# Optimization experiments

Measured on AMD Instinct MI355X. Metric: run time of the kernel, lower is better.

Reference implementation:

```python
import jax, jax.numpy as jnp
import numpy as np

N, E = 50000, 800000
D, H, C, ED = 128, 8, 16, 32  # in_channels, heads, head_dim, edge_dim
EPS = 1e-5

def _ln(x, g, b):
    mu = jnp.mean(x, axis=-1, keepdims=True)
    var = jnp.mean((x - mu) ** 2, axis=-1, keepdims=True)
    return (x - mu) * jax.lax.rsqrt(var + EPS) * g + b

def setup_inputs() -> dict:
    key = jax.random.key(0)
    ks = jax.random.split(key, 20)
    s = 0.05
    inp = {
        'x': jax.random.normal(ks[0], (N, D), jnp.float32),
        'edge_index': jax.random.randint(ks[1], (2, E), 0, N, jnp.int64),
        'edge_attr': jax.random.normal(ks[2], (E, ED), jnp.float32),
        'Wq': jax.random.normal(ks[3], (D, H * C)) * s,
        'bq': jnp.zeros((H * C,)),
        'Wk': jax.random.normal(ks[4], (D, H * C)) * s,
        'bk': jnp.zeros((H * C,)),
        'Wv': jax.random.normal(ks[5], (D, H * C)) * s,
        'bv': jnp.zeros((H * C,)),
        'We': jax.random.normal(ks[6], (ED, H * C)) * s,
        'Wskip': jax.random.normal(ks[7], (D, H * C)) * s,
        'bskip': jnp.zeros((H * C,)),
        'ln1_g': jnp.ones((D,)), 'ln1_b': jnp.zeros((D,)),
        'W1': jax.random.normal(ks[8], (D, 4 * D)) * s,
        'b1': jnp.zeros((4 * D,)),
        'W2': jax.random.normal(ks[9], (4 * D, D)) * s,
        'b2': jnp.zeros((D,)),
        'ln2_g': jnp.ones((D,)), 'ln2_b': jnp.zeros((D,)),
    }
    return inp

def reference(x, edge_index, edge_attr, Wq, bq, Wk, bk, Wv, bv, We, Wskip, bskip,
              ln1_g, ln1_b, W1, b1, W2, b2, ln2_g, ln2_b):
    src, dst = edge_index[0], edge_index[1]
    # node-level projections, then gather per-edge  [N,H,C] -> [E,H,C]
    q = (x @ Wq + bq).reshape(N, H, C)
    k = (x @ Wk + bk).reshape(N, H, C)
    v = (x @ Wv + bv).reshape(N, H, C)
    e = (edge_attr @ We).reshape(E, H, C)
    k_e = k[src] + e
    alpha = jnp.sum(q[dst] * k_e, axis=-1) / jnp.sqrt(jnp.float32(C))  # [E,H]
    # segment softmax over destination nodes
    m = jax.ops.segment_max(alpha, dst, num_segments=N)               # [N,H]
    p = jnp.exp(alpha - m[dst])
    denom = jax.ops.segment_sum(p, dst, num_segments=N)
    a = p / (denom[dst] + 1e-16)
    out_e = (v[src] + e) * a[..., None]                               # [E,H,C]
    attn = jax.ops.segment_sum(out_e, dst, num_segments=N).reshape(N, H * C)
    attn = attn + x @ Wskip + bskip  # root/skip connection
    # transformer block: residual + LN + FFN + LN (dropout = identity, eval)
    h = _ln(x + attn, ln1_g, ln1_b)
    ffn = jax.nn.relu(h @ W1 + b1) @ W2 + b2
    return _ln(h + ffn, ln2_g, ln2_b)
```

## Files before the change

### kernel.cpp

```cpp
#include <hip/hip_runtime.h>
#include <hip/hip_bf16.h>

using bf16 = __hip_bfloat16;
typedef __attribute__((ext_vector_type(8))) short short8;
typedef __attribute__((ext_vector_type(4))) float floatx4;

#define NN 50000
#define EE 800000
#define DD 128
#define HH 8
#define CC 16
#define EDD 32
#define DF 512
#define NQC 64
#define PART 782

__device__ __forceinline__ float b2f(bf16 v) { return __bfloat162float(v); }
__device__ __forceinline__ float bs2f(short s) {
    bf16 h = *reinterpret_cast<bf16*>(&s);
    return __bfloat162float(h);
}
__device__ __forceinline__ float bu2f(unsigned short s) {
    unsigned int u = ((unsigned int)s) << 16;
    return *reinterpret_cast<float*>(&u);
}
__device__ __forceinline__ short f2bs(float v) {
    bf16 h = __float2bfloat16(v);
    return *reinterpret_cast<short*>(&h);
}

__global__ void k_detect(const int* __restrict__ ei, int* __restrict__ flag)
{
    if (threadIdx.x == 0 && blockIdx.x == 0) {
        int all0 = 1;
        for (int i = 0; i < 16; ++i) all0 &= (ei[2 * i + 1] == 0);
        flag[0] = all0;
    }
}

__device__ __forceinline__ int clampn(int v)
{
    return (v < 0) ? 0 : (v >= NN ? NN - 1 : v);
}

__global__ void k_packall(const float* __restrict__ Wq, const float* __restrict__ Wk,
                          const float* __restrict__ Wv, const float* __restrict__ Wsk,
                          const float* __restrict__ W1, const float* __restrict__ W2,
                          const float* __restrict__ We,
                          bf16* __restrict__ wqp, bf16* __restrict__ wkp,
                          bf16* __restrict__ wvp, bf16* __restrict__ wskp,
                          bf16* __restrict__ w1p, bf16* __restrict__ w2p,
                          bf16* __restrict__ wep)
{
    int idx = blockIdx.x * 256 + threadIdx.x;
    const float* W; bf16* out; int ksteps, N, local;
    if (idx < 65536) {
        int wsel = idx >> 14; local = idx & 16383;
        W   = (wsel == 0) ? Wq  : (wsel == 1) ? Wk  : (wsel == 2) ? Wv  : Wsk;
        out = (wsel == 0) ? wqp : (wsel == 1) ? wkp : (wsel == 2) ? wvp : wskp;
        ksteps = 4; N = 128;
    } else if (idx < 131072) { local = idx - 65536;  W = W1; out = w1p; ksteps = 4;  N = 512; }
    else if (idx < 196608)   { local = idx - 131072; W = W2; out = w2p; ksteps = 16; N = 128; }
    else if (idx < 200704)   { local = idx - 196608; W = We; out = wep; ksteps = 1;  N = 128; }
    else return;
    int j = local & 7, lane = (local >> 3) & 63, rest = local >> 9;
    int kstep = rest % ksteps, ntile = rest / ksteps;
    int quad = lane >> 4, m = lane & 15;
    int k = kstep * 32 + quad * 8 + j;
    int n = ntile * 16 + m;
    out[local] = __float2bfloat16(W[(size_t)k * N + n]);
}

__global__ __launch_bounds__(256) void k_proj(
    const float* __restrict__ x,
    const bf16* __restrict__ wqp, const bf16* __restrict__ wkp,
    const bf16* __restrict__ wvp, const bf16* __restrict__ wskp,
    const float* __restrict__ bq, const float* __restrict__ bk,
    const float* __restrict__ bv, const float* __restrict__ bsk,
    bf16* __restrict__ qb, unsigned int* __restrict__ kvb,
    bf16* __restrict__ skipb)
{
    __shared__ __align__(16) short xs[32][136];
    __shared__ __align__(16) short os[32][520];
    const int t = threadIdx.x;
    const int wave = t >> 6, lane = t & 63;
    const int quad = lane >> 4, m = lane & 15;
    const int n0 = blockIdx.x * 32;

    for (int idx = t; idx < 32 * 32; idx += 256) {
        int row = idx >> 5, g = idx & 31;
        int node = n0 + row;
        float4 xv = {0.f, 0.f, 0.f, 0.f};
        if (node < NN) xv = *reinterpret_cast<const float4*>(&x[(size_t)node * 128 + g * 4]);
        short4 s4;
        s4.x = f2bs(xv.x); s4.y = f2bs(xv.y); s4.z = f2bs(xv.z); s4.w = f2bs(xv.w);
        *reinterpret_cast<short4*>(&xs[row][g * 4]) = s4;
    }
    __syncthreads();

    const bf16* Wp = (wave == 0) ? wqp : (wave == 1) ? wkp : (wave == 2) ? wvp : wskp;
    const float* bias = (wave == 0) ? bq : (wave == 1) ? bk : (wave == 2) ? bv : bsk;

    floatx4 acc[2][8];
#pragma unroll
    for (int mt = 0; mt < 2; ++mt)
#pragma unroll
        for (int nt = 0; nt < 8; ++nt) acc[mt][nt] = (floatx4){0.f, 0.f, 0.f, 0.f};

#pragma unroll
    for (int kstep = 0; kstep < 4; ++kstep) {
        short8 af0 = *reinterpret_cast<const short8*>(&xs[m][kstep * 32 + quad * 8]);
        short8 af1 = *reinterpret_cast<const short8*>(&xs[16 + m][kstep * 32 + quad * 8]);
#pragma unroll
        for (int nt = 0; nt < 8; ++nt) {
            short8 bf = *reinterpret_cast<const short8*>(
                reinterpret_cast<const short*>(Wp) + ((nt * 4 + kstep) * 64 + lane) * 8);
            acc[0][nt] = __builtin_amdgcn_mfma_f32_16x16x32_bf16(af0, bf, acc[0][nt], 0, 0, 0);
            acc[1][nt] = __builtin_amdgcn_mfma_f32_16x16x32_bf16(af1, bf, acc[1][nt], 0, 0, 0);
        }
    }
#pragma unroll
    for (int nt = 0; nt < 8; ++nt) {
        float bs = bias[nt * 16 + m];
#pragma unroll
        for (int mt = 0; mt < 2; ++mt)
#pragma unroll
            for (int r = 0; r < 4; ++r)
                os[mt * 16 + quad * 4 + r][wave * 128 + nt * 16 + m] = f2bs(acc[mt][nt][r] + bs);
    }
    __syncthreads();
    for (int idx = t; idx < 32 * 64; idx += 256) {
        int row = idx >> 6, c = idx & 63;
        int node = n0 + row;
        if (node >= NN) continue;
        unsigned int qu  = *reinterpret_cast<const unsigned int*>(&os[row][2 * c]);
        unsigned int ku  = *reinterpret_cast<const unsigned int*>(&os[row][128 + 2 * c]);
        unsigned int vu  = *reinterpret_cast<const unsigned int*>(&os[row][256 + 2 * c]);
        unsigned int sku = *reinterpret_cast<const unsigned int*>(&os[row][384 + 2 * c]);
        reinterpret_cast<unsigned int*>(qb)[(size_t)node * 64 + c] = qu;
        reinterpret_cast<unsigned int*>(skipb)[(size_t)node * 64 + c] = sku;
        uint2 kv;
        kv.x = (ku & 0xffffu) | (vu << 16);
        kv.y = (ku >> 16) | (vu & 0xffff0000u);
        reinterpret_cast<uint2*>(kvb)[(size_t)node * 64 + c] = kv;
    }
}

__global__ void k_hist(const int* __restrict__ ei, const int* __restrict__ flag,
                       int* __restrict__ deg)
{
    int tt = blockIdx.x * 256 + threadIdx.x;
    int i0 = tt * 2;
    if (i0 >= EE) return;
    int d0, d1;
    if (flag[0]) {
        int4 v = *reinterpret_cast<const int4*>(&ei[2 * EE + 2 * i0]);
        d0 = v.x; d1 = v.z;
    } else {
        int2 v = *reinterpret_cast<const int2*>(&ei[EE + i0]);
        d0 = v.x; d1 = v.y;
    }
    atomicAdd(&deg[clampn(d0)], 1);
    atomicAdd(&deg[clampn(d1)], 1);
}

__global__ __launch_bounds__(1024) void k_scan(const int* __restrict__ deg,
                                               int* __restrict__ rowstart)
{
    __shared__ int s[1024];
    const int t = threadIdx.x;
    const int CH = 49;
    int base = t * CH;
    int sum = 0;
    for (int i = 0; i < CH; i++) {
        int idx = base + i;
        if (idx < NN) sum += deg[idx];
    }
    s[t] = sum;
    __syncthreads();
    int own = sum;
    for (int off = 1; off < 1024; off <<= 1) {
        int v = (t >= off) ? s[t - off] : 0;
        __syncthreads();
        s[t] += v;
        __syncthreads();
    }
    int run = s[t] - own;
    for (int i = 0; i < CH; i++) {
        int idx = base + i;
        if (idx < NN) {
            rowstart[idx] = run;
            run += deg[idx];
        }
    }
    if (t == 0) rowstart[NN] = EE;
}

__global__ void k_scatter(const int* __restrict__ ei, const int* __restrict__ flag,
                          const int* __restrict__ rowstart,
                          int* __restrict__ cursor, int* __restrict__ srcs,
                          const float* __restrict__ ea,
                          short* __restrict__ eacsr)
{
    int i = blockIdx.x * 256 + threadIdx.x;
    if (i >= EE) return;
    int is64 = flag[0];
    int d = clampn(is64 ? ei[2 * EE + 2 * i] : ei[EE + i]);
    int s = clampn(is64 ? ei[2 * i] : ei[i]);
    int pos = rowstart[d] + atomicAdd(&cursor[d], 1);
    srcs[pos] = s;
    const float4* er = reinterpret_cast<const float4*>(ea + (size_t)i * 32);
    short8* dst = reinterpret_cast<short8*>(eacsr + (size_t)pos * 32);
#pragma unroll
    for (int g = 0; g < 4; ++g) {
        float4 a = er[2 * g], b = er[2 * g + 1];
        short8 o;
        o[0] = f2bs(a.x); o[1] = f2bs(a.y); o[2] = f2bs(a.z); o[3] = f2bs(a.w);
        o[4] = f2bs(b.x); o[5] = f2bs(b.y); o[6] = f2bs(b.z); o[7] = f2bs(b.w);
        dst[g] = o;
    }
}

__global__ __launch_bounds__(256) void k_attn(
    const float* __restrict__ x,
    const short* __restrict__ eacsr, const bf16* __restrict__ wep,
    const bf16* __restrict__ qb, const unsigned int* __restrict__ kvb,
    const bf16* __restrict__ skipb,
    const int* __restrict__ rowstart, const int* __restrict__ srcs,
    const float* __restrict__ ln1g, const float* __restrict__ ln1b,
    int* __restrict__ qcounter, bf16* __restrict__ hb)
{
    __shared__ __align__(16) short es[4][128][18];
    __shared__ __align__(16) short wes[4096];
    const int t = threadIdx.x;
    const int wave = t >> 6, lane = t & 63;
    const int quad = lane >> 4, m = lane & 15;

    for (int idx = t; idx < 512; idx += 256)
        *reinterpret_cast<short8*>(&wes[idx * 8]) =
            *reinterpret_cast<const short8*>(reinterpret_cast<const short*>(wep) + idx * 8);
    __syncthreads();

    short (*esw)[18] = es[wave];
    const float QS = 0.3606737602f;

    const int gw = blockIdx.x * 4 + wave;
    const int c  = gw & (NQC - 1);
    const int base = c * PART;
    const int cnt_c = (NN - base < PART) ? (NN - base) : PART;
    int* qc = qcounter + c * 16;

    for (;;) {
        int nl;
        if (lane == 0) nl = atomicAdd(qc, 1);
        nl = __builtin_amdgcn_readfirstlane(nl);
        if (nl >= cnt_c) break;
        const int n = base + nl;

        unsigned int qp = reinterpret_cast<const unsigned int*>(qb)[(size_t)n * 64 + lane];
        float q0 = bu2f((unsigned short)(qp & 0xffffu)) * QS;
        float q1 = bu2f((unsigned short)(qp >> 16)) * QS;

        const int eoff = rowstart[n], eend = rowstart[n + 1];
        float lsum = 0.f, acc0 = 0.f, acc1 = 0.f;

        for (int p0 = eoff; p0 < eend; p0 += 16) {
            int pos = p0 + m;
            int pc = (pos < eend) ? pos : eoff;
            int sj_all = srcs[pc];

            short8 Af = *reinterpret_cast<const short8*>(eacsr + (size_t)pc * 32 + quad * 8);

            uint2 kvr[16];
#pragma unroll
            for (int j = 0; j < 16; ++j) {
                int sj = __builtin_amdgcn_readlane(sj_all, j);
                kvr[j] = reinterpret_cast<const uint2*>(kvb + (size_t)(unsigned)sj * 128)[lane];
            }

#pragma unroll
            for (int nt = 0; nt < 8; ++nt) {
                short8 Bf = *reinterpret_cast<const short8*>(&wes[(nt * 64 + lane) * 8]);
                floatx4 C = {0.f, 0.f, 0.f, 0.f};
                C = __builtin_amdgcn_mfma_f32_16x16x32_bf16(Af, Bf, C, 0, 0, 0);
                int col = nt * 16 + m;
                unsigned int d0 = (unsigned int)(unsigned short)f2bs(C[0]) |
                                  ((unsigned int)(unsigned short)f2bs(C[1]) << 16);
                unsigned int d1 = (unsigned int)(unsigned short)f2bs(C[2]) |
                                  ((unsigned int)(unsigned short)f2bs(C[3]) << 16);
                unsigned int* p = reinterpret_cast<unsigned int*>(&esw[col][quad * 4]);
                p[0] = d0; p[1] = d1;
            }
            __builtin_amdgcn_wave_barrier();

            unsigned int ea[8], eb[8];
            {
                const unsigned int* ra = reinterpret_cast<const unsigned int*>(&esw[2 * lane][0]);
                const unsigned int* rb = reinterpret_cast<const unsigned int*>(&esw[2 * lane + 1][0]);
#pragma unroll
                for (int jj = 0; jj < 8; ++jj) { ea[jj] = ra[jj]; eb[jj] = rb[jj]; }
            }

            int cnt = eend - p0; if (cnt > 16) cnt = 16;
#pragma unroll
            for (int j = 0; j < 16; ++j) {
                unsigned int eva = ea[j >> 1], evb = eb[j >> 1];
                float e0 = (j & 1) ? bu2f((unsigned short)(eva >> 16))
                                   : bu2f((unsigned short)(eva & 0xffffu));
                float e1 = (j & 1) ? bu2f((unsigned short)(evb >> 16))
                                   : bu2f((unsigned short)(evb & 0xffffu));
                float k0 = bu2f((unsigned short)(kvr[j].x & 0xffffu));
                float v0 = bu2f((unsigned short)(kvr[j].x >> 16));
                float k1 = bu2f((unsigned short)(kvr[j].y & 0xffffu));
                float v1 = bu2f((unsigned short)(kvr[j].y >> 16));
                float pr = fmaf(k1 + e1, q1, (k0 + e0) * q0);
                pr += __shfl_xor(pr, 1);
                pr += __shfl_xor(pr, 2);
                pr += __shfl_xor(pr, 4);
                float w = (j < cnt) ? __builtin_amdgcn_exp2f(pr) : 0.f;
                lsum += w;
                acc0 = fmaf(v0 + e0, w, acc0);
                acc1 = fmaf(v1 + e1, w, acc1);
            }
            __builtin_amdgcn_wave_barrier();
        }

        float rden = 1.f / (lsum + 1e-16f);
        float attn0 = acc0 * rden, attn1 = acc1 * rden;
        float2 xv = *reinterpret_cast<const float2*>(x + (size_t)n * 128 + 2 * lane);
        unsigned int skp = reinterpret_cast<const unsigned int*>(skipb)[(size_t)n * 64 + lane];
        float pre0 = xv.x + attn0 + bu2f((unsigned short)(skp & 0xffffu));
        float pre1 = xv.y + attn1 + bu2f((unsigned short)(skp >> 16));
        float s1 = pre0 + pre1, s2 = pre0 * pre0 + pre1 * pre1;
#pragma unroll
        for (int off = 1; off < 64; off <<= 1) {
            s1 += __shfl_xor(s1, off);
            s2 += __shfl_xor(s2, off);
        }
        float mu = s1 * (1.f / 128.f);
        float var = s2 * (1.f / 128.f) - mu * mu;
        float inv = rsqrtf(var + 1e-5f);
        float2 g  = *reinterpret_cast<const float2*>(ln1g + 2 * lane);
        float2 bb = *reinterpret_cast<const float2*>(ln1b + 2 * lane);
        float h0 = (pre0 - mu) * inv * g.x + bb.x;
        float h1 = (pre1 - mu) * inv * g.y + bb.y;
        unsigned int hu = (unsigned int)(unsigned short)f2bs(h0) |
                          ((unsigned int)(unsigned short)f2bs(h1) << 16);
        reinterpret_cast<unsigned int*>(hb)[(size_t)n * 64 + lane] = hu;
    }
}

__global__ __launch_bounds__(256) void k_ffn(
    const bf16* __restrict__ hb,
    const bf16* __restrict__ w1p, const float* __restrict__ b1,
    const bf16* __restrict__ w2p, const float* __restrict__ b2,
    const float* __restrict__ ln2g, const float* __restrict__ ln2b,
    float* __restrict__ out)
{
    __shared__ __align__(16) short hs[32][136];
    __shared__ __align__(16) short t1s[32][520];
    float* fs = reinterpret_cast<float*>(&t1s[0][0]);
    const int t = threadIdx.x;
    const int wave = t >> 6, lane = t & 63;
    const int quad = lane >> 4, m = lane & 15;
    const int n0 = blockIdx.x * 32;

    for (int idx = t; idx < 32 * 16; idx += 256) {
        int row = idx >> 4, g = idx & 15;
        int node = n0 + row;
        if (node < NN) {
            *reinterpret_cast<float4*>(&hs[row][g * 8]) =
                *reinterpret_cast<const float4*>(&hb[(size_t)node * 128 + g * 8]);
        } else {
            float4 z = {0.f, 0.f, 0.f, 0.f};
            *reinterpret_cast<float4*>(&hs[row][g * 8]) = z;
        }
    }
    __syncthreads();

    floatx4 acc1[2][8];
#pragma unroll
    for (int mt = 0; mt < 2; ++mt)
#pragma unroll
        for (int nt = 0; nt < 8; ++nt) acc1[mt][nt] = (floatx4){0.f, 0.f, 0.f, 0.f};
#pragma unroll
    for (int kstep = 0; kstep < 4; ++kstep) {
        short8 af0 = *reinterpret_cast<const short8*>(&hs[m][kstep * 32 + quad * 8]);
        short8 af1 = *reinterpret_cast<const short8*>(&hs[16 + m][kstep * 32 + quad * 8]);
#pragma unroll
        for (int nt = 0; nt < 8; ++nt) {
            short8 bf = *reinterpret_cast<const short8*>(
                reinterpret_cast<const short*>(w1p) + (((wave * 8 + nt) * 4 + kstep) * 64 + lane) * 8);
            acc1[0][nt] = __builtin_amdgcn_mfma_f32_16x16x32_bf16(af0, bf, acc1[0][nt], 0, 0, 0);
            acc1[1][nt] = __builtin_amdgcn_mfma_f32_16x16x32_bf16(af1, bf, acc1[1][nt], 0, 0, 0);
        }
    }
#pragma unroll
    for (int nt = 0; nt < 8; ++nt) {
        float bs = b1[wave * 128 + nt * 16 + m];
#pragma unroll
        for (int mt = 0; mt < 2; ++mt)
#pragma unroll
            for (int r = 0; r < 4; ++r)
                t1s[mt * 16 + quad * 4 + r][wave * 128 + nt * 16 + m] =
                    f2bs(fmaxf(acc1[mt][nt][r] + bs, 0.f));
    }
    __syncthreads();

    floatx4 acc2[2][2];
#pragma unroll
    for (int mt = 0; mt < 2; ++mt)
#pragma unroll
        for (int nt = 0; nt < 2; ++nt) acc2[mt][nt] = (floatx4){0.f, 0.f, 0.f, 0.f};
#pragma unroll
    for (int kstep = 0; kstep < 16; ++kstep) {
        short8 af0 = *reinterpret_cast<const short8*>(&t1s[m][kstep * 32 + quad * 8]);
        short8 af1 = *reinterpret_cast<const short8*>(&t1s[16 + m][kstep * 32 + quad * 8]);
#pragma unroll
        for (int nt = 0; nt < 2; ++nt) {
            short8 bf = *reinterpret_cast<const short8*>(
                reinterpret_cast<const short*>(w2p) + (((wave * 2 + nt) * 16 + kstep) * 64 + lane) * 8);
            acc2[0][nt] = __builtin_amdgcn_mfma_f32_16x16x32_bf16(af0, bf, acc2[0][nt], 0, 0, 0);
            acc2[1][nt] = __builtin_amdgcn_mfma_f32_16x16x32_bf16(af1, bf, acc2[1][nt], 0, 0, 0);
        }
    }
    __syncthreads();
#pragma unroll
    for (int nt = 0; nt < 2; ++nt) {
        int col = (wave * 2 + nt) * 16 + m;
        float bs = b2[col];
#pragma unroll
        for (int mt = 0; mt < 2; ++mt)
#pragma unroll
            for (int r = 0; r < 4; ++r)
                fs[(mt * 16 + quad * 4 + r) * 132 + col] = acc2[mt][nt][r] + bs;
    }
    __syncthreads();

    for (int rr = 0; rr < 8; ++rr) {
        int row = wave * 8 + rr;
        int node = n0 + row;
        float p0 = bs2f(hs[row][lane]) + fs[row * 132 + lane];
        float p1 = bs2f(hs[row][lane + 64]) + fs[row * 132 + lane + 64];
        float s1 = p0 + p1, s2 = p0 * p0 + p1 * p1;
#pragma unroll
        for (int off = 1; off < 64; off <<= 1) {
            s1 += __shfl_xor(s1, off);
            s2 += __shfl_xor(s2, off);
        }
        float mu = s1 * (1.f / 128.f);
        float var = s2 * (1.f / 128.f) - mu * mu;
        float inv = rsqrtf(var + 1e-5f);
        if (node < NN) {
            out[(size_t)node * 128 + lane] = (p0 - mu) * inv * ln2g[lane] + ln2b[lane];
            out[(size_t)node * 128 + lane + 64] = (p1 - mu) * inv * ln2g[lane + 64] + ln2b[lane + 64];
        }
    }
}

extern "C" void kernel_launch(void* const* d_in, const int* in_sizes, int n_in,
                              void* d_out, int out_size, void* d_ws, size_t ws_size,
                              hipStream_t stream)
{
    const float* x    = (const float*)d_in[0];
    const int*   ei   = (const int*)d_in[1];
    const float* ea   = (const float*)d_in[2];
    const float* Wq   = (const float*)d_in[3];
    const float* bq   = (const float*)d_in[4];
    const float* Wk   = (const float*)d_in[5];
    const float* bk   = (const float*)d_in[6];
    const float* Wv   = (const float*)d_in[7];
    const float* bv   = (const float*)d_in[8];
    const float* We   = (const float*)d_in[9];
    const float* Wsk  = (const float*)d_in[10];
    const float* bsk  = (const float*)d_in[11];
    const float* ln1g = (const float*)d_in[12];
    const float* ln1b = (const float*)d_in[13];
    const float* W1   = (const float*)d_in[14];
    const float* b1   = (const float*)d_in[15];
    const float* W2   = (const float*)d_in[16];
    const float* b2   = (const float*)d_in[17];
    const float* ln2g = (const float*)d_in[18];
    const float* ln2b = (const float*)d_in[19];

    char* ws = (char*)d_ws;
    size_t off = 0;
    auto alloc = [&](size_t bytes) -> void* {
        void* p = ws + off;
        off += (bytes + 255) & ~(size_t)255;
        return p;
    };
    int*   flag     = (int*)alloc(256);
    int*   qcounter = (int*)alloc((size_t)NQC * 16 * 4);
    int*   deg      = (int*)alloc((size_t)NN * 4);
    int*   cursor   = (int*)alloc((size_t)NN * 4);
    int*   rowstart = (int*)alloc((size_t)(NN + 1) * 4);
    int*   srcs     = (int*)alloc((size_t)EE * 4);
    short* eacsr    = (short*)alloc((size_t)EE * 32 * 2);
    bf16*  qb       = (bf16*)alloc((size_t)NN * 128 * 2);
    unsigned int* kvb = (unsigned int*)alloc((size_t)NN * 128 * 4);
    bf16*  skipb    = (bf16*)alloc((size_t)NN * 128 * 2);
    bf16*  hb       = (bf16*)alloc((size_t)NN * 128 * 2);
    bf16*  wqp      = (bf16*)alloc((size_t)16384 * 2);
    bf16*  wkp      = (bf16*)alloc((size_t)16384 * 2);
    bf16*  wvp      = (bf16*)alloc((size_t)16384 * 2);
    bf16*  wskp     = (bf16*)alloc((size_t)16384 * 2);
    bf16*  w1p      = (bf16*)alloc((size_t)65536 * 2);
    bf16*  w2p      = (bf16*)alloc((size_t)65536 * 2);
    bf16*  wep      = (bf16*)alloc((size_t)4096 * 2);

    hipMemsetAsync(deg, 0, (size_t)NN * 4, stream);
    hipMemsetAsync(cursor, 0, (size_t)NN * 4, stream);
    hipMemsetAsync(qcounter, 0, (size_t)NQC * 16 * 4, stream);

    k_detect<<<1, 64, 0, stream>>>(ei, flag);
    k_packall<<<(200704 + 255) / 256, 256, 0, stream>>>(
        Wq, Wk, Wv, Wsk, W1, W2, We, wqp, wkp, wvp, wskp, w1p, w2p, wep);
    k_hist<<<(EE / 2 + 255) / 256, 256, 0, stream>>>(ei, flag, deg);
    k_proj<<<(NN + 31) / 32, 256, 0, stream>>>(x, wqp, wkp, wvp, wskp,
                                               bq, bk, bv, bsk, qb, kvb, skipb);
    k_scan<<<1, 1024, 0, stream>>>(deg, rowstart);
    k_scatter<<<(EE + 255) / 256, 256, 0, stream>>>(ei, flag, rowstart, cursor,
                                                    srcs, ea, eacsr);
    k_attn<<<1536, 256, 0, stream>>>(x, eacsr, wep, qb, kvb, skipb,
                                     rowstart, srcs, ln1g, ln1b, qcounter, hb);
    k_ffn<<<(NN + 31) / 32, 256, 0, stream>>>(hb, w1p, b1, w2p, b2, ln2g, ln2b, (float*)d_out);
}
```

Measured before the change: 564.3 us.

## Fuse detect into pack kernel, batch attention node grabs, use nontemporal stores

Moves the edge-index dtype detection into the weight pack kernel, dropping one kernel launch. The attention kernel now claims four nodes per atomic instead of one, which cuts contention on the per-chunk work counter. The head-reduction shuffles are replaced with ds_swizzle. Nontemporal stores are used for the CSR scatter and for the final output writes. Coarser node grabs may worsen load balance at the tail, and nontemporal stores can hurt if the scattered data is reread soon while still in cache.

```diff
diff --git a/kernel.cpp b/kernel.cpp
--- a/kernel.cpp
+++ b/kernel.cpp
@@ -29,15 +29,6 @@
     return *reinterpret_cast<short*>(&h);
 }
 
-__global__ void k_detect(const int* __restrict__ ei, int* __restrict__ flag)
-{
-    if (threadIdx.x == 0 && blockIdx.x == 0) {
-        int all0 = 1;
-        for (int i = 0; i < 16; ++i) all0 &= (ei[2 * i + 1] == 0);
-        flag[0] = all0;
-    }
-}
-
 __device__ __forceinline__ int clampn(int v)
 {
     return (v < 0) ? 0 : (v >= NN ? NN - 1 : v);
@@ -50,7 +41,8 @@
                           bf16* __restrict__ wqp, bf16* __restrict__ wkp,
                           bf16* __restrict__ wvp, bf16* __restrict__ wskp,
                           bf16* __restrict__ w1p, bf16* __restrict__ w2p,
-                          bf16* __restrict__ wep)
+                          bf16* __restrict__ wep,
+                          const int* __restrict__ ei, int* __restrict__ flag)
 {
     int idx = blockIdx.x * 256 + threadIdx.x;
     const float* W; bf16* out; int ksteps, N, local;
@@ -62,7 +54,14 @@
     } else if (idx < 131072) { local = idx - 65536;  W = W1; out = w1p; ksteps = 4;  N = 512; }
     else if (idx < 196608)   { local = idx - 131072; W = W2; out = w2p; ksteps = 16; N = 128; }
     else if (idx < 200704)   { local = idx - 196608; W = We; out = wep; ksteps = 1;  N = 128; }
-    else return;
+    else {
+        if (idx == 200704) {
+            int all0 = 1;
+            for (int i = 0; i < 16; ++i) all0 &= (ei[2 * i + 1] == 0);
+            flag[0] = all0;
+        }
+        return;
+    }
     int j = local & 7, lane = (local >> 3) & 63, rest = local >> 9;
     int kstep = rest % ksteps, ntile = rest / ksteps;
     int quad = lane >> 4, m = lane & 15;
@@ -208,7 +207,7 @@
     int d = clampn(is64 ? ei[2 * EE + 2 * i] : ei[EE + i]);
     int s = clampn(is64 ? ei[2 * i] : ei[i]);
     int pos = rowstart[d] + atomicAdd(&cursor[d], 1);
-    srcs[pos] = s;
+    __builtin_nontemporal_store(s, &srcs[pos]);
     const float4* er = reinterpret_cast<const float4*>(ea + (size_t)i * 32);
     short8* dst = reinterpret_cast<short8*>(eacsr + (size_t)pos * 32);
 #pragma unroll
@@ -217,7 +216,7 @@
         short8 o;
         o[0] = f2bs(a.x); o[1] = f2bs(a.y); o[2] = f2bs(a.z); o[3] = f2bs(a.w);
         o[4] = f2bs(b.x); o[5] = f2bs(b.y); o[6] = f2bs(b.z); o[7] = f2bs(b.w);
-        dst[g] = o;
+        __builtin_nontemporal_store(o, &dst[g]);
     }
 }
 
@@ -252,101 +251,105 @@
 
     for (;;) {
         int nl;
-        if (lane == 0) nl = atomicAdd(qc, 1);
+        if (lane == 0) nl = atomicAdd(qc, 4);
         nl = __builtin_amdgcn_readfirstlane(nl);
         if (nl >= cnt_c) break;
-        const int n = base + nl;
-
-        unsigned int qp = reinterpret_cast<const unsigned int*>(qb)[(size_t)n * 64 + lane];
-        float q0 = bu2f((unsigned short)(qp & 0xffffu)) * QS;
-        float q1 = bu2f((unsigned short)(qp >> 16)) * QS;
-
-        const int eoff = rowstart[n], eend = rowstart[n + 1];
-        float lsum = 0.f, acc0 = 0.f, acc1 = 0.f;
-
-        for (int p0 = eoff; p0 < eend; p0 += 16) {
-            int pos = p0 + m;
-            int pc = (pos < eend) ? pos : eoff;
-            int sj_all = srcs[pc];
-
-            short8 Af = *reinterpret_cast<const short8*>(eacsr + (size_t)pc * 32 + quad * 8);
-
-            uint2 kvr[16];
-#pragma unroll
-            for (int j = 0; j < 16; ++j) {
-                int sj = __builtin_amdgcn_readlane(sj_all, j);
-                kvr[j] = reinterpret_cast<const uint2*>(kvb + (size_t)(unsigned)sj * 128)[lane];
+        const int nhi = (nl + 4 < cnt_c) ? nl + 4 : cnt_c;
+
+        for (int ni = nl; ni < nhi; ++ni) {
+            const int n = base + ni;
+
+            unsigned int qp = reinterpret_cast<const unsigned int*>(qb)[(size_t)n * 64 + lane];
+            float q0 = bu2f((unsigned short)(qp & 0xffffu)) * QS;
+            float q1 = bu2f((unsigned short)(qp >> 16)) * QS;
+
+            const int eoff = rowstart[n], eend = rowstart[n + 1];
+            float lsum = 0.f, acc0 = 0.f, acc1 = 0.f;
+
+            for (int p0 = eoff; p0 < eend; p0 += 16) {
+                int pos = p0 + m;
+                int pc = (pos < eend) ? pos : eoff;
+                int sj_all = srcs[pc];
+
+                short8 Af = *reinterpret_cast<const short8*>(eacsr + (size_t)pc * 32 + quad * 8);
+
+                uint2 kvr[16];
+#pragma unroll
+                for (int j = 0; j < 16; ++j) {
+                    int sj = __builtin_amdgcn_readlane(sj_all, j);
+                    kvr[j] = reinterpret_cast<const uint2*>(kvb + (size_t)(unsigned)sj * 128)[lane];
+                }
+
+#pragma unroll
+                for (int nt = 0; nt < 8; ++nt) {
+                    short8 Bf = *reinterpret_cast<const short8*>(&wes[(nt * 64 + lane) * 8]);
+                    floatx4 C = {0.f, 0.f, 0.f, 0.f};
+                    C = __builtin_amdgcn_mfma_f32_16x16x32_bf16(Af, Bf, C, 0, 0, 0);
+                    int col = nt * 16 + m;
+                    unsigned int d0 = (unsigned int)(unsigned short)f2bs(C[0]) |
+                                      ((unsigned int)(unsigned short)f2bs(C[1]) << 16);
+                    unsigned int d1 = (unsigned int)(unsigned short)f2bs(C[2]) |
+                                      ((unsigned int)(unsigned short)f2bs(C[3]) << 16);
+                    unsigned int* p = reinterpret_cast<unsigned int*>(&esw[col][quad * 4]);
+                    p[0] = d0; p[1] = d1;
+                }
+                __builtin_amdgcn_wave_barrier();
+
+                unsigned int ear[8], ebr[8];
+                {
+                    const unsigned int* ra = reinterpret_cast<const unsigned int*>(&esw[2 * lane][0]);
+                    const unsigned int* rb = reinterpret_cast<const unsigned int*>(&esw[2 * lane + 1][0]);
+#pragma unroll
+                    for (int jj = 0; jj < 8; ++jj) { ear[jj] = ra[jj]; ebr[jj] = rb[jj]; }
+                }
+
+                int cnt = eend - p0; if (cnt > 16) cnt = 16;
+#pragma unroll
+                for (int j = 0; j < 16; ++j) {
+                    unsigned int eva = ear[j >> 1], evb = ebr[j >> 1];
+                    float e0 = (j & 1) ? bu2f((unsigned short)(eva >> 16))
+                                       : bu2f((unsigned short)(eva & 0xffffu));
+                    float e1 = (j & 1) ? bu2f((unsigned short)(evb >> 16))
+                                       : bu2f((unsigned short)(evb & 0xffffu));
+                    float k0 = bu2f((unsigned short)(kvr[j].x & 0xffffu));
+                    float v0 = bu2f((unsigned short)(kvr[j].x >> 16));
+                    float k1 = bu2f((unsigned short)(kvr[j].y & 0xffffu));
+                    float v1 = bu2f((unsigned short)(kvr[j].y >> 16));
+                    float pr = fmaf(k1 + e1, q1, (k0 + e0) * q0);
+                    pr += __int_as_float(__builtin_amdgcn_ds_swizzle(__float_as_int(pr), 0x041F));
+                    pr += __int_as_float(__builtin_amdgcn_ds_swizzle(__float_as_int(pr), 0x081F));
+                    pr += __int_as_float(__builtin_amdgcn_ds_swizzle(__float_as_int(pr), 0x101F));
+                    float w = (j < cnt) ? __builtin_amdgcn_exp2f(pr) : 0.f;
+                    lsum += w;
+                    acc0 = fmaf(v0 + e0, w, acc0);
+                    acc1 = fmaf(v1 + e1, w, acc1);
+                }
+                __builtin_amdgcn_wave_barrier();
             }
 
-#pragma unroll
-            for (int nt = 0; nt < 8; ++nt) {
-                short8 Bf = *reinterpret_cast<const short8*>(&wes[(nt * 64 + lane) * 8]);
-                floatx4 C = {0.f, 0.f, 0.f, 0.f};
-                C = __builtin_amdgcn_mfma_f32_16x16x32_bf16(Af, Bf, C, 0, 0, 0);
-                int col = nt * 16 + m;
-                unsigned int d0 = (unsigned int)(unsigned short)f2bs(C[0]) |
-                                  ((unsigned int)(unsigned short)f2bs(C[1]) << 16);
-                unsigned int d1 = (unsigned int)(unsigned short)f2bs(C[2]) |
-                                  ((unsigned int)(unsigned short)f2bs(C[3]) << 16);
-                unsigned int* p = reinterpret_cast<unsigned int*>(&esw[col][quad * 4]);
-                p[0] = d0; p[1] = d1;
+            float rden = 1.f / (lsum + 1e-16f);
+            float attn0 = acc0 * rden, attn1 = acc1 * rden;
+            float2 xv = *reinterpret_cast<const float2*>(x + (size_t)n * 128 + 2 * lane);
+            unsigned int skp = reinterpret_cast<const unsigned int*>(skipb)[(size_t)n * 64 + lane];
+            float pre0 = xv.x + attn0 + bu2f((unsigned short)(skp & 0xffffu));
+            float pre1 = xv.y + attn1 + bu2f((unsigned short)(skp >> 16));
+            float s1 = pre0 + pre1, s2 = pre0 * pre0 + pre1 * pre1;
+#pragma unroll
+            for (int off = 1; off < 64; off <<= 1) {
+                s1 += __shfl_xor(s1, off);
+                s2 += __shfl_xor(s2, off);
             }
-            __builtin_amdgcn_wave_barrier();
-
-            unsigned int ea[8], eb[8];
-            {
-                const unsigned int* ra = reinterpret_cast<const unsigned int*>(&esw[2 * lane][0]);
-                const unsigned int* rb = reinterpret_cast<const unsigned int*>(&esw[2 * lane + 1][0]);
-#pragma unroll
-                for (int jj = 0; jj < 8; ++jj) { ea[jj] = ra[jj]; eb[jj] = rb[jj]; }
-            }
-
-            int cnt = eend - p0; if (cnt > 16) cnt = 16;
-#pragma unroll
-            for (int j = 0; j < 16; ++j) {
-                unsigned int eva = ea[j >> 1], evb = eb[j >> 1];
-                float e0 = (j & 1) ? bu2f((unsigned short)(eva >> 16))
-                                   : bu2f((unsigned short)(eva & 0xffffu));
-                float e1 = (j & 1) ? bu2f((unsigned short)(evb >> 16))
-                                   : bu2f((unsigned short)(evb & 0xffffu));
-                float k0 = bu2f((unsigned short)(kvr[j].x & 0xffffu));
-                float v0 = bu2f((unsigned short)(kvr[j].x >> 16));
-                float k1 = bu2f((unsigned short)(kvr[j].y & 0xffffu));
-                float v1 = bu2f((unsigned short)(kvr[j].y >> 16));
-                float pr = fmaf(k1 + e1, q1, (k0 + e0) * q0);
-                pr += __shfl_xor(pr, 1);
-                pr += __shfl_xor(pr, 2);
-                pr += __shfl_xor(pr, 4);
-                float w = (j < cnt) ? __builtin_amdgcn_exp2f(pr) : 0.f;
-                lsum += w;
-                acc0 = fmaf(v0 + e0, w, acc0);
-                acc1 = fmaf(v1 + e1, w, acc1);
-            }
-            __builtin_amdgcn_wave_barrier();
-        }
-
-        float rden = 1.f / (lsum + 1e-16f);
-        float attn0 = acc0 * rden, attn1 = acc1 * rden;
-        float2 xv = *reinterpret_cast<const float2*>(x + (size_t)n * 128 + 2 * lane);
-        unsigned int skp = reinterpret_cast<const unsigned int*>(skipb)[(size_t)n * 64 + lane];
-        float pre0 = xv.x + attn0 + bu2f((unsigned short)(skp & 0xffffu));
-        float pre1 = xv.y + attn1 + bu2f((unsigned short)(skp >> 16));
-        float s1 = pre0 + pre1, s2 = pre0 * pre0 + pre1 * pre1;
-#pragma unroll
-        for (int off = 1; off < 64; off <<= 1) {
-            s1 += __shfl_xor(s1, off);
-            s2 += __shfl_xor(s2, off);
-        }
-        float mu = s1 * (1.f / 128.f);
-        float var = s2 * (1.f / 128.f) - mu * mu;
-        float inv = rsqrtf(var + 1e-5f);
-        float2 g  = *reinterpret_cast<const float2*>(ln1g + 2 * lane);
-        float2 bb = *reinterpret_cast<const float2*>(ln1b + 2 * lane);
-        float h0 = (pre0 - mu) * inv * g.x + bb.x;
-        float h1 = (pre1 - mu) * inv * g.y + bb.y;
-        unsigned int hu = (unsigned int)(unsigned short)f2bs(h0) |
-                          ((unsigned int)(unsigned short)f2bs(h1) << 16);
-        reinterpret_cast<unsigned int*>(hb)[(size_t)n * 64 + lane] = hu;
+            float mu = s1 * (1.f / 128.f);
+            float var = s2 * (1.f / 128.f) - mu * mu;
+            float inv = rsqrtf(var + 1e-5f);
+            float2 g  = *reinterpret_cast<const float2*>(ln1g + 2 * lane);
+            float2 bb = *reinterpret_cast<const float2*>(ln1b + 2 * lane);
+            float h0 = (pre0 - mu) * inv * g.x + bb.x;
+            float h1 = (pre1 - mu) * inv * g.y + bb.y;
+            unsigned int hu = (unsigned int)(unsigned short)f2bs(h0) |
+                              ((unsigned int)(unsigned short)f2bs(h1) << 16);
+            reinterpret_cast<unsigned int*>(hb)[(size_t)n * 64 + lane] = hu;
+        }
     }
 }
 
@@ -452,8 +455,10 @@
         float var = s2 * (1.f / 128.f) - mu * mu;
         float inv = rsqrtf(var + 1e-5f);
         if (node < NN) {
-            out[(size_t)node * 128 + lane] = (p0 - mu) * inv * ln2g[lane] + ln2b[lane];
-            out[(size_t)node * 128 + lane + 64] = (p1 - mu) * inv * ln2g[lane + 64] + ln2b[lane + 64];
+            float o0 = (p0 - mu) * inv * ln2g[lane] + ln2b[lane];
+            float o1 = (p1 - mu) * inv * ln2g[lane + 64] + ln2b[lane + 64];
+            __builtin_nontemporal_store(o0, &out[(size_t)node * 128 + lane]);
+            __builtin_nontemporal_store(o1, &out[(size_t)node * 128 + lane + 64]);
         }
     }
 }
@@ -513,9 +518,8 @@
     hipMemsetAsync(cursor, 0, (size_t)NN * 4, stream);
     hipMemsetAsync(qcounter, 0, (size_t)NQC * 16 * 4, stream);
 
-    k_detect<<<1, 64, 0, stream>>>(ei, flag);
-    k_packall<<<(200704 + 255) / 256, 256, 0, stream>>>(
-        Wq, Wk, Wv, Wsk, W1, W2, We, wqp, wkp, wvp, wskp, w1p, w2p, wep);
+    k_packall<<<785, 256, 0, stream>>>(
+        Wq, Wk, Wv, Wsk, W1, W2, We, wqp, wkp, wvp, wskp, w1p, w2p, wep, ei, flag);
     k_hist<<<(EE / 2 + 255) / 256, 256, 0, stream>>>(ei, flag, deg);
     k_proj<<<(NN + 31) / 32, 256, 0, stream>>>(x, wqp, wkp, wvp, wskp,
                                                bq, bk, bv, bsk, qb, kvb, skipb);
```

Result: slower. 634.4 us (+12.4%).
